# Kernel optimization log

Measured on AMD Instinct MI355X. Metric: run time of the kernel, lower is better.

The kernel has to match this reference:

```python
import jax, jax.numpy as jnp
import numpy as np

HC = 4           # hc_mult
ITERS = 20       # hc_sinkhorn_iters
EPS = 1e-6       # hc_eps
NORM_EPS = 1e-6  # rms_norm_eps


def setup_inputs() -> dict:
    key = jax.random.key(0)
    k = jax.random.split(key, 4)
    B, S, H = 1, 4096, 4096
    mix = (2 + HC) * HC  # 24
    hidden_states = jax.random.normal(k[0], (B, S, HC, H), jnp.float32)
    hc_fn = jax.random.normal(k[1], (mix, HC * H), jnp.float32) * 0.02
    hc_base = jax.random.normal(k[2], (mix,), jnp.float32) * 0.02
    hc_scale = jnp.ones((3,), jnp.float32)
    norm_weight = jnp.ones((H,), jnp.float32)
    w_inner = jax.random.normal(k[3], (H, H), jnp.float32) * 0.02
    return {
        "hidden_states": hidden_states,
        "hc_fn": hc_fn,
        "hc_base": hc_base,
        "hc_scale": hc_scale,
        "norm_weight": norm_weight,
        "w_inner": w_inner,
    }


def reference(hidden_states, hc_fn, hc_base, hc_scale, norm_weight, w_inner):
    B, S, hc, H = hidden_states.shape
    # RMS stat over the flattened (hc*H) feature dim
    flat = hidden_states.reshape(B, S, hc * H).astype(jnp.float32)
    rs = jax.lax.rsqrt(jnp.mean(jnp.square(flat), axis=-1, keepdims=True) + NORM_EPS)
    mixes = jnp.einsum('bsd,md->bsm', flat, hc_fn) * rs  # [B,S,(2+hc)*hc]

    ps, qs, cs = hc_scale[0], hc_scale[1], hc_scale[2]
    pre = jax.nn.sigmoid(mixes[..., :hc] * ps + hc_base[:hc]) + EPS           # [B,S,hc]
    post = jax.nn.sigmoid(mixes[..., hc:2 * hc] * qs + hc_base[hc:2 * hc]) + EPS
    comb = jax.nn.sigmoid(
        mixes[..., 2 * hc:].reshape(B, S, hc, hc) * cs
        + hc_base[2 * hc:].reshape(hc, hc)
    ) + EPS  # [B,S,hc,hc]

    # 20-iter Sinkhorn row/column normalization
    def sink(_, c):
        c = c / (jnp.sum(c, axis=-1, keepdims=True) + EPS)
        return c / (jnp.sum(c, axis=-2, keepdims=True) + EPS)
    comb = jax.lax.fori_loop(0, ITERS, sink, comb)

    # weighted stream reduction -> [B,S,H]
    reduced = jnp.einsum('bsh,bshd->bsd', pre, hidden_states)

    # norm + inner sub-block (RMSNorm then dense projection)
    nr = jax.lax.rsqrt(jnp.mean(jnp.square(reduced), axis=-1, keepdims=True) + NORM_EPS)
    normed = reduced * nr * norm_weight
    out = jnp.einsum('bsd,ed->bse', normed, w_inner)  # [B,S,H]

    # broadcast back to streams: post-gated write + Sinkhorn-mixed residual
    expanded = post[..., None] * out[:, :, None, :] \
        + jnp.einsum('bshk,bskd->bshd', comb, hidden_states)
    return expanded.astype(hidden_states.dtype)
```

## Files before the change

kernel.cpp:

```cpp
#include <hip/hip_runtime.h>
#include <math.h>

#define S_DIM 4096
#define H_DIM 4096
#define HC_N 4
#define HD_DIM 16384
#define MIXN 24
#define SINK_IT 20

typedef float f32x4 __attribute__((ext_vector_type(4)));
typedef __bf16 bf16x8 __attribute__((ext_vector_type(8)));
typedef unsigned short u16x8 __attribute__((ext_vector_type(8)));
typedef unsigned short u16x4 __attribute__((ext_vector_type(4)));

__device__ __forceinline__ unsigned short f2bf(float f) {
  unsigned u = __builtin_bit_cast(unsigned, f);
  u += 0x7FFFu + ((u >> 16) & 1u);
  return (unsigned short)(u >> 16);
}
__device__ __forceinline__ float bf2f(unsigned short h) {
  return __builtin_bit_cast(float, (unsigned)h << 16);
}

__global__ __launch_bounds__(256) void k_w2bf(const float* __restrict__ w,
                                              unsigned short* __restrict__ wb) {
  const size_t i = (size_t)(blockIdx.x * 256 + threadIdx.x) * 8;
  f32x4 a = *(const f32x4*)(w + i);
  f32x4 b = *(const f32x4*)(w + i + 4);
  u16x8 o;
  o[0] = f2bf(a.x); o[1] = f2bf(a.y); o[2] = f2bf(a.z); o[3] = f2bf(a.w);
  o[4] = f2bf(b.x); o[5] = f2bf(b.y); o[6] = f2bf(b.z); o[7] = f2bf(b.w);
  *(u16x8*)(wb + i) = o;
}

__global__ __launch_bounds__(256) void k_mixes(const float* __restrict__ hs,
                                               const float* __restrict__ fn,
                                               float* __restrict__ mixraw,
                                               float* __restrict__ sumsq) {
  __shared__ __align__(16) float lds[HC_N][1024];
  const int tid = threadIdx.x;
  const int b = blockIdx.x;
  const int lane = tid & 63, wave = tid >> 6;
  const int mbase = wave * 6;

  float acc[HC_N][6];
  float ss[HC_N];
#pragma unroll
  for (int r = 0; r < HC_N; r++) {
    ss[r] = 0.f;
#pragma unroll
    for (int j = 0; j < 6; j++) acc[r][j] = 0.f;
  }

  const size_t rowbase = (size_t)b * HC_N * HD_DIM;
  for (int it = 0; it < 16; ++it) {
    __syncthreads();
#pragma unroll
    for (int r = 0; r < HC_N; r++) {
      f32x4 v = *(const f32x4*)(hs + rowbase + (size_t)r * HD_DIM + it * 1024 + tid * 4);
      *(f32x4*)(&lds[r][tid * 4]) = v;
    }
    __syncthreads();
#pragma unroll
    for (int ii = 0; ii < 4; ii++) {
      const int c4 = ii * 64 + lane;
      f32x4 h4[HC_N];
#pragma unroll
      for (int r = 0; r < HC_N; r++) h4[r] = *(const f32x4*)(&lds[r][c4 * 4]);
      if (wave == 0) {
#pragma unroll
        for (int r = 0; r < HC_N; r++)
          ss[r] += h4[r].x * h4[r].x + h4[r].y * h4[r].y + h4[r].z * h4[r].z + h4[r].w * h4[r].w;
      }
#pragma unroll
      for (int j = 0; j < 6; j++) {
        f32x4 fv = *(const f32x4*)(fn + (size_t)(mbase + j) * HD_DIM + it * 1024 + c4 * 4);
#pragma unroll
        for (int r = 0; r < HC_N; r++)
          acc[r][j] += h4[r].x * fv.x + h4[r].y * fv.y + h4[r].z * fv.z + h4[r].w * fv.w;
      }
    }
  }

#pragma unroll
  for (int r = 0; r < HC_N; r++) {
#pragma unroll
    for (int j = 0; j < 6; j++) {
      float v = acc[r][j];
#pragma unroll
      for (int off = 32; off >= 1; off >>= 1) v += __shfl_xor(v, off, 64);
      if (lane == 0) mixraw[(size_t)(b * 4 + r) * MIXN + mbase + j] = v;
    }
  }
  if (wave == 0) {
#pragma unroll
    for (int r = 0; r < HC_N; r++) {
      float v = ss[r];
#pragma unroll
      for (int off = 32; off >= 1; off >>= 1) v += __shfl_xor(v, off, 64);
      if (lane == 0) sumsq[b * 4 + r] = v;
    }
  }
}

__global__ __launch_bounds__(256) void k_gates(const float* __restrict__ mixraw,
                                               const float* __restrict__ sumsq,
                                               const float* __restrict__ hbase,
                                               const float* __restrict__ hscale,
                                               float* __restrict__ gates) {
  const int row = blockIdx.x * 256 + threadIdx.x;
  const float rs = rsqrtf(sumsq[row] * (1.0f / HD_DIM) + 1e-6f);
  const float ps = hscale[0], qs = hscale[1], cs = hscale[2];
  const float* mr = mixraw + (size_t)row * MIXN;
  float g[MIXN];
#pragma unroll
  for (int m = 0; m < MIXN; m++) {
    const float sc = (m < 4) ? ps : ((m < 8) ? qs : cs);
    const float x = mr[m] * rs * sc + hbase[m];
    g[m] = 1.0f / (1.0f + expf(-x)) + 1e-6f;
  }
  for (int t = 0; t < SINK_IT; t++) {
#pragma unroll
    for (int i = 0; i < 4; i++) {
      const float s = g[8 + i * 4 + 0] + g[8 + i * 4 + 1] + g[8 + i * 4 + 2] + g[8 + i * 4 + 3] + 1e-6f;
#pragma unroll
      for (int j = 0; j < 4; j++) g[8 + i * 4 + j] /= s;
    }
#pragma unroll
    for (int j = 0; j < 4; j++) {
      const float s = g[8 + 0 + j] + g[8 + 4 + j] + g[8 + 8 + j] + g[8 + 12 + j] + 1e-6f;
#pragma unroll
      for (int i = 0; i < 4; i++) g[8 + i * 4 + j] /= s;
    }
  }
  float* go = gates + (size_t)row * MIXN;
#pragma unroll
  for (int m = 0; m < MIXN; m++) go[m] = g[m];
}

__global__ __launch_bounds__(256) void k_reduce_norm(const float* __restrict__ hs,
                                                     const float* __restrict__ gates,
                                                     const float* __restrict__ nw,
                                                     unsigned short* __restrict__ normed) {
  const int s = blockIdx.x, tid = threadIdx.x;
  const int lane = tid & 63, wave = tid >> 6;
  const float* g = gates + (size_t)s * MIXN;
  const float p0 = g[0], p1 = g[1], p2 = g[2], p3 = g[3];
  const size_t base = (size_t)s * HC_N * H_DIM;

  f32x4 red[4];
  float ssq = 0.f;
#pragma unroll
  for (int it = 0; it < 4; ++it) {
    const int d4 = it * 256 + tid;
    f32x4 a = *(const f32x4*)(hs + base + (size_t)0 * H_DIM + (size_t)d4 * 4);
    f32x4 b = *(const f32x4*)(hs + base + (size_t)1 * H_DIM + (size_t)d4 * 4);
    f32x4 c = *(const f32x4*)(hs + base + (size_t)2 * H_DIM + (size_t)d4 * 4);
    f32x4 d = *(const f32x4*)(hs + base + (size_t)3 * H_DIM + (size_t)d4 * 4);
    f32x4 v = p0 * a + p1 * b + p2 * c + p3 * d;
    red[it] = v;
    ssq += v.x * v.x + v.y * v.y + v.z * v.z + v.w * v.w;
  }
#pragma unroll
  for (int off = 32; off >= 1; off >>= 1) ssq += __shfl_xor(ssq, off, 64);
  __shared__ float ls[4];
  if (lane == 0) ls[wave] = ssq;
  __syncthreads();
  const float tot = ls[0] + ls[1] + ls[2] + ls[3];
  const float nr = rsqrtf(tot * (1.0f / H_DIM) + 1e-6f);
#pragma unroll
  for (int it = 0; it < 4; ++it) {
    const int d4 = it * 256 + tid;
    f32x4 w = *(const f32x4*)(nw + (size_t)d4 * 4);
    f32x4 v = red[it] * nr;
    v = v * w;
    u16x4 o;
    o[0] = f2bf(v.x); o[1] = f2bf(v.y); o[2] = f2bf(v.z); o[3] = f2bf(v.w);
    *(u16x4*)(normed + (size_t)s * H_DIM + (size_t)d4 * 4) = o;
  }
}

__device__ __forceinline__ void gload_lds16(const unsigned short* g, unsigned short* l) {
  __builtin_amdgcn_global_load_lds(
      (const __attribute__((address_space(1))) unsigned int*)(const void*)g,
      (__attribute__((address_space(3))) unsigned int*)(void*)l, 16, 0, 0);
}

#define GEMM_NT 128

__global__ __launch_bounds__(512, 2) void k_gemm(const unsigned short* __restrict__ A,
                                                 const unsigned short* __restrict__ B,
                                                 unsigned short* __restrict__ C) {
  __shared__ __align__(16) unsigned short sA[4][256 * 32];
  __shared__ __align__(16) unsigned short sB[4][256 * 32];
  const int tid = threadIdx.x;
  const int lane = tid & 63, wave = tid >> 6;

  const int bid = blockIdx.x;
  const int v = bid & 7, u = bid >> 3;
  const int bm = u & 15, bn = v * 2 + (u >> 4);
  const int wm = wave >> 2, wn = wave & 3;

  const int srow = lane >> 2;
  const int sk = (lane & 3) * 8;
  const unsigned short* ga = A + (size_t)(bm * 256 + wave * 32 + srow) * 4096 + sk;
  const unsigned short* gb = B + (size_t)(bn * 256 + wave * 32 + srow) * 4096 + sk;
  const int ldst0 = wave * 1024 + lane * 8;
  const int ldst1 = ldst0 + 512;

#define STAGE(slot, t) do {                                        \
    const unsigned short* gha = ga + (size_t)(t) * 32;             \
    const unsigned short* ghb = gb + (size_t)(t) * 32;             \
    gload_lds16(gha,             &sA[(slot)][ldst0]);              \
    gload_lds16(gha + 16 * 4096, &sA[(slot)][ldst1]);              \
    gload_lds16(ghb,             &sB[(slot)][ldst0]);              \
    gload_lds16(ghb + 16 * 4096, &sB[(slot)][ldst1]);              \
  } while (0)

  f32x4 acc[8][4];
  f32x4 zero = {0.f, 0.f, 0.f, 0.f};
#pragma unroll
  for (int mf = 0; mf < 8; mf++)
#pragma unroll
    for (int nf = 0; nf < 4; nf++) acc[mf][nf] = zero;

  const int frow = lane & 15, fk = (lane >> 4) * 8;
  const int abase = wm * 128 + frow;
  const int bbase = wn * 64 + frow;

#define COMPUTE(slot) do {                                                    \
    bf16x8 af[8], bfr[4];                                                     \
    _Pragma("unroll") for (int mf = 0; mf < 8; mf++)                          \
      af[mf] = *(const bf16x8*)&sA[(slot)][(abase + mf * 16) * 32 + fk];      \
    _Pragma("unroll") for (int nf = 0; nf < 4; nf++)                          \
      bfr[nf] = *(const bf16x8*)&sB[(slot)][(bbase + nf * 16) * 32 + fk];     \
    __builtin_amdgcn_s_setprio(1);                                            \
    _Pragma("unroll") for (int mf = 0; mf < 8; mf++)                          \
      _Pragma("unroll") for (int nf = 0; nf < 4; nf++)                        \
        acc[mf][nf] = __builtin_amdgcn_mfma_f32_16x16x32_bf16(af[mf], bfr[nf], acc[mf][nf], 0, 0, 0); \
    __builtin_amdgcn_s_setprio(0);                                            \
  } while (0)

  STAGE(0, 0);
  STAGE(1, 1);
  STAGE(2, 2);
  asm volatile("s_waitcnt vmcnt(8)" ::: "memory");
  asm volatile("s_barrier" ::: "memory");

  for (int t = 0; t < GEMM_NT - 3; ++t) {
    STAGE((t + 3) & 3, t + 3);
    COMPUTE(t & 3);
    asm volatile("s_waitcnt vmcnt(8)" ::: "memory");
    asm volatile("s_barrier" ::: "memory");
  }
  COMPUTE((GEMM_NT - 3) & 3);
  asm volatile("s_waitcnt vmcnt(4)" ::: "memory");
  asm volatile("s_barrier" ::: "memory");
  COMPUTE((GEMM_NT - 2) & 3);
  asm volatile("s_waitcnt vmcnt(0)" ::: "memory");
  asm volatile("s_barrier" ::: "memory");
  COMPUTE((GEMM_NT - 1) & 3);

#undef STAGE
#undef COMPUTE

  const int crow0 = bm * 256 + wm * 128 + (lane >> 4) * 4;
  const int ccol0 = bn * 256 + wn * 64 + (lane & 15);
#pragma unroll
  for (int mf = 0; mf < 8; mf++)
#pragma unroll
    for (int nf = 0; nf < 4; nf++)
#pragma unroll
      for (int j = 0; j < 4; j++)
        C[(size_t)(crow0 + mf * 16 + j) * 4096 + ccol0 + nf * 16] = f2bf(acc[mf][nf][j]);
}

__global__ __launch_bounds__(256) void k_expand(const float* __restrict__ hs,
                                                const unsigned short* __restrict__ outb,
                                                const float* __restrict__ gates,
                                                float* __restrict__ y) {
  const int s = blockIdx.x, tid = threadIdx.x;
  const float* g = gates + (size_t)s * MIXN;
  float post[4], cb[4][4];
#pragma unroll
  for (int h = 0; h < 4; h++) post[h] = g[4 + h];
#pragma unroll
  for (int h = 0; h < 4; h++)
#pragma unroll
    for (int k = 0; k < 4; k++) cb[h][k] = g[8 + h * 4 + k];

  const size_t base = (size_t)s * HC_N * H_DIM;
#pragma unroll
  for (int it = 0; it < 4; ++it) {
    const int d4 = it * 256 + tid;
    f32x4 hv[4];
#pragma unroll
    for (int k = 0; k < 4; k++)
      hv[k] = *(const f32x4*)(hs + base + (size_t)k * H_DIM + (size_t)d4 * 4);
    u16x4 ob = *(const u16x4*)(outb + (size_t)s * H_DIM + (size_t)d4 * 4);
    f32x4 o = {bf2f(ob[0]), bf2f(ob[1]), bf2f(ob[2]), bf2f(ob[3])};
#pragma unroll
    for (int h = 0; h < 4; h++) {
      f32x4 e = post[h] * o + cb[h][0] * hv[0] + cb[h][1] * hv[1] + cb[h][2] * hv[2] + cb[h][3] * hv[3];
      *(f32x4*)(y + base + (size_t)h * H_DIM + (size_t)d4 * 4) = e;
    }
  }
}

extern "C" void kernel_launch(void* const* d_in, const int* in_sizes, int n_in,
                              void* d_out, int out_size, void* d_ws, size_t ws_size,
                              hipStream_t stream) {
  const float* hs = (const float*)d_in[0];
  const float* fn = (const float*)d_in[1];
  const float* hbase = (const float*)d_in[2];
  const float* hscale = (const float*)d_in[3];
  const float* nw = (const float*)d_in[4];
  const float* wi = (const float*)d_in[5];
  float* y = (float*)d_out;

  char* ws = (char*)d_ws;
  float* mixraw = (float*)(ws);
  float* sumsq = (float*)(ws + 393216);
  float* gates = (float*)(ws + 409600);
  unsigned short* normed = (unsigned short*)(ws + 1048576);
  unsigned short* wb = (unsigned short*)(ws + 1048576 + 33554432);
  unsigned short* outb = (unsigned short*)(ws + 1048576 + 2 * 33554432);

  k_w2bf<<<8192, 256, 0, stream>>>(wi, wb);
  k_mixes<<<1024, 256, 0, stream>>>(hs, fn, mixraw, sumsq);
  k_gates<<<16, 256, 0, stream>>>(mixraw, sumsq, hbase, hscale, gates);
  k_reduce_norm<<<4096, 256, 0, stream>>>(hs, gates, nw, normed);
  k_gemm<<<256, 512, 0, stream>>>(normed, wb, outb);
  k_expand<<<4096, 256, 0, stream>>>(hs, outb, gates, y);
}
```

Measured before the change: 487.1 us.

## Restructure GEMM main loop into 8-phase ping-pong schedule with interleaved loads

Result: no change. 490.4 us (+0.7%).

```diff
diff --git a/kernel.cpp b/kernel.cpp
--- a/kernel.cpp
+++ b/kernel.cpp
@@ -186,13 +186,14 @@
       (__attribute__((address_space(3))) unsigned int*)(void*)l, 16, 0, 0);
 }
 
-#define GEMM_NT 128
+#define VMW(n) asm volatile("s_waitcnt vmcnt(" #n ")" ::: "memory")
+#define BAR    asm volatile("s_barrier" ::: "memory")
 
 __global__ __launch_bounds__(512, 2) void k_gemm(const unsigned short* __restrict__ A,
                                                  const unsigned short* __restrict__ B,
                                                  unsigned short* __restrict__ C) {
-  __shared__ __align__(16) unsigned short sA[4][256 * 32];
-  __shared__ __align__(16) unsigned short sB[4][256 * 32];
+  __shared__ __align__(16) unsigned short sAbuf[2][2][256 * 32];
+  __shared__ __align__(16) unsigned short sBbuf[2][2][256 * 32];
   const int tid = threadIdx.x;
   const int lane = tid & 63, wave = tid >> 6;
 
@@ -202,20 +203,11 @@
   const int wm = wave >> 2, wn = wave & 3;
 
   const int srow = lane >> 2;
-  const int sk = (lane & 3) * 8;
-  const unsigned short* ga = A + (size_t)(bm * 256 + wave * 32 + srow) * 4096 + sk;
-  const unsigned short* gb = B + (size_t)(bn * 256 + wave * 32 + srow) * 4096 + sk;
-  const int ldst0 = wave * 1024 + lane * 8;
-  const int ldst1 = ldst0 + 512;
-
-#define STAGE(slot, t) do {                                        \
-    const unsigned short* gha = ga + (size_t)(t) * 32;             \
-    const unsigned short* ghb = gb + (size_t)(t) * 32;             \
-    gload_lds16(gha,             &sA[(slot)][ldst0]);              \
-    gload_lds16(gha + 16 * 4096, &sA[(slot)][ldst1]);              \
-    gload_lds16(ghb,             &sB[(slot)][ldst0]);              \
-    gload_lds16(ghb + 16 * 4096, &sB[(slot)][ldst1]);              \
-  } while (0)
+  const int sk8 = (lane & 3) * 8;
+  const unsigned short* gA = A + (size_t)(bm * 256 + wave * 32 + srow) * 4096 + sk8;
+  const unsigned short* gB = B + (size_t)(bn * 256 + wave * 32 + srow) * 4096 + sk8;
+  const int ld0 = wave * 1024 + lane * 8;
+  const int ld1 = ld0 + 512;
 
   f32x4 acc[8][4];
   f32x4 zero = {0.f, 0.f, 0.f, 0.f};
@@ -223,46 +215,63 @@
   for (int mf = 0; mf < 8; mf++)
 #pragma unroll
     for (int nf = 0; nf < 4; nf++) acc[mf][nf] = zero;
+  bf16x8 af[8];
 
   const int frow = lane & 15, fk = (lane >> 4) * 8;
-  const int abase = wm * 128 + frow;
-  const int bbase = wn * 64 + frow;
-
-#define COMPUTE(slot) do {                                                    \
-    bf16x8 af[8], bfr[4];                                                     \
-    _Pragma("unroll") for (int mf = 0; mf < 8; mf++)                          \
-      af[mf] = *(const bf16x8*)&sA[(slot)][(abase + mf * 16) * 32 + fk];      \
-    _Pragma("unroll") for (int nf = 0; nf < 4; nf++)                          \
-      bfr[nf] = *(const bf16x8*)&sB[(slot)][(bbase + nf * 16) * 32 + fk];     \
-    __builtin_amdgcn_s_setprio(1);                                            \
-    _Pragma("unroll") for (int mf = 0; mf < 8; mf++)                          \
-      _Pragma("unroll") for (int nf = 0; nf < 4; nf++)                        \
-        acc[mf][nf] = __builtin_amdgcn_mfma_f32_16x16x32_bf16(af[mf], bfr[nf], acc[mf][nf], 0, 0, 0); \
-    __builtin_amdgcn_s_setprio(0);                                            \
+
+#define PHASE_BODY(db, kh, nh, dostg, sdst, gsrc, t, skh) do {                  \
+    if ((nh) == 0) {                                                            \
+      _Pragma("unroll") for (int mf = 0; mf < 8; mf++)                          \
+        af[mf] = *(const bf16x8*)&sAbuf[db][kh][(wm * 128 + mf * 16 + frow) * 32 + fk]; \
+    }                                                                           \
+    bf16x8 b0 = *(const bf16x8*)&sBbuf[db][kh][(wn * 64 + ((nh) * 2 + 0) * 16 + frow) * 32 + fk]; \
+    bf16x8 b1 = *(const bf16x8*)&sBbuf[db][kh][(wn * 64 + ((nh) * 2 + 1) * 16 + frow) * 32 + fk]; \
+    if (dostg) {                                                                \
+      const unsigned short* _g = (gsrc) + (size_t)(t) * 64 + (skh) * 32;        \
+      gload_lds16(_g,              (sdst) + ld0);                               \
+      gload_lds16(_g + 16 * 4096,  (sdst) + ld1);                               \
+    }                                                                           \
+    BAR;                                                                        \
+    __builtin_amdgcn_s_setprio(1);                                              \
+    _Pragma("unroll") for (int mf = 0; mf < 8; mf++) {                          \
+      acc[mf][(nh) * 2 + 0] = __builtin_amdgcn_mfma_f32_16x16x32_bf16(af[mf], b0, acc[mf][(nh) * 2 + 0], 0, 0, 0); \
+      acc[mf][(nh) * 2 + 1] = __builtin_amdgcn_mfma_f32_16x16x32_bf16(af[mf], b1, acc[mf][(nh) * 2 + 1], 0, 0, 0); \
+    }                                                                           \
+    __builtin_amdgcn_s_setprio(0);                                              \
   } while (0)
 
-  STAGE(0, 0);
-  STAGE(1, 1);
-  STAGE(2, 2);
-  asm volatile("s_waitcnt vmcnt(8)" ::: "memory");
-  asm volatile("s_barrier" ::: "memory");
-
-  for (int t = 0; t < GEMM_NT - 3; ++t) {
-    STAGE((t + 3) & 3, t + 3);
-    COMPUTE(t & 3);
-    asm volatile("s_waitcnt vmcnt(8)" ::: "memory");
-    asm volatile("s_barrier" ::: "memory");
-  }
-  COMPUTE((GEMM_NT - 3) & 3);
-  asm volatile("s_waitcnt vmcnt(4)" ::: "memory");
-  asm volatile("s_barrier" ::: "memory");
-  COMPUTE((GEMM_NT - 2) & 3);
-  asm volatile("s_waitcnt vmcnt(0)" ::: "memory");
-  asm volatile("s_barrier" ::: "memory");
-  COMPUTE((GEMM_NT - 1) & 3);
-
-#undef STAGE
-#undef COMPUTE
+  gload_lds16(gA,                  &sAbuf[0][0][0] + ld0);
+  gload_lds16(gA + 16 * 4096,      &sAbuf[0][0][0] + ld1);
+  gload_lds16(gB,                  &sBbuf[0][0][0] + ld0);
+  gload_lds16(gB + 16 * 4096,      &sBbuf[0][0][0] + ld1);
+  gload_lds16(gA + 32,             &sAbuf[0][1][0] + ld0);
+  gload_lds16(gA + 32 + 16 * 4096, &sAbuf[0][1][0] + ld1);
+  gload_lds16(gB + 32,             &sBbuf[0][1][0] + ld0);
+  gload_lds16(gB + 32 + 16 * 4096, &sBbuf[0][1][0] + ld1);
+  VMW(4);
+  BAR;
+
+  for (int i = 0; i < 31; ++i) {
+    const int t1 = 2 * i + 1, t2 = 2 * i + 2;
+    PHASE_BODY(0, 0, 0, 1, &sAbuf[1][0][0], gA, t1, 0);          BAR;
+    PHASE_BODY(0, 0, 1, 1, &sBbuf[1][0][0], gB, t1, 0); VMW(4);  BAR;
+    PHASE_BODY(0, 1, 0, 1, &sAbuf[1][1][0], gA, t1, 1);          BAR;
+    PHASE_BODY(0, 1, 1, 1, &sBbuf[1][1][0], gB, t1, 1); VMW(4);  BAR;
+    PHASE_BODY(1, 0, 0, 1, &sAbuf[0][0][0], gA, t2, 0);          BAR;
+    PHASE_BODY(1, 0, 1, 1, &sBbuf[0][0][0], gB, t2, 0); VMW(4);  BAR;
+    PHASE_BODY(1, 1, 0, 1, &sAbuf[0][1][0], gA, t2, 1);          BAR;
+    PHASE_BODY(1, 1, 1, 1, &sBbuf[0][1][0], gB, t2, 1); VMW(4);  BAR;
+  }
+  PHASE_BODY(0, 0, 0, 1, &sAbuf[1][0][0], gA, 63, 0);            BAR;
+  PHASE_BODY(0, 0, 1, 1, &sBbuf[1][0][0], gB, 63, 0); VMW(4);    BAR;
+  PHASE_BODY(0, 1, 0, 1, &sAbuf[1][1][0], gA, 63, 1);            BAR;
+  PHASE_BODY(0, 1, 1, 1, &sBbuf[1][1][0], gB, 63, 1); VMW(0);    BAR;
+  PHASE_BODY(1, 0, 0, 0, &sAbuf[0][0][0], gA, 0, 0);             BAR;
+  PHASE_BODY(1, 0, 1, 0, &sAbuf[0][0][0], gA, 0, 0);             BAR;
+  PHASE_BODY(1, 1, 0, 0, &sAbuf[0][0][0], gA, 0, 0);             BAR;
+  PHASE_BODY(1, 1, 1, 0, &sAbuf[0][0][0], gA, 0, 0);
+
+#undef PHASE_BODY
 
   const int crow0 = bm * 256 + wm * 128 + (lane >> 4) * 4;
   const int ccol0 = bn * 256 + wn * 64 + (lane & 15);
```
